# Performance work log

Hardware: AMD Instinct MI355X
Metric: run time of the kernel (lower is better)

The kernel has to match this reference:

```python
import jax, jax.numpy as jnp
import numpy as np

N = 131072   # nodes (flattened batch)
SI, VI = 128, 64   # in_dims
SO, VO = 128, 64   # out_dims
HD = 128           # h_dim


def setup_inputs() -> dict:
    key = jax.random.key(0)
    ks = jax.random.split(key, 8)
    scale = lambda fan_in: 1.0 / np.sqrt(fan_in)
    return {
        "s": jax.random.normal(ks[0], (N, SI), dtype=jnp.float32),
        "V": jax.random.normal(ks[1], (N, VI, 3), dtype=jnp.float32),
        # Linear(vi, h_dim, bias=False): weight [h_dim, vi]
        "W_h": jax.random.uniform(ks[2], (HD, VI), jnp.float32, -scale(VI), scale(VI)),
        # Linear(h_dim, vo, bias=False): weight [vo, h_dim]
        "W_V": jax.random.uniform(ks[3], (VO, HD), jnp.float32, -scale(HD), scale(HD)),
        # Linear(si + h_dim, so)
        "W_s_w": jax.random.uniform(ks[4], (SO, SI + HD), jnp.float32, -scale(SI + HD), scale(SI + HD)),
        "W_s_b": jax.random.uniform(ks[5], (SO,), jnp.float32, -scale(SI + HD), scale(SI + HD)),
        # Linear(so, vo) gate
        "W_g_w": jax.random.uniform(ks[6], (VO, SO), jnp.float32, -scale(SO), scale(SO)),
        "W_g_b": jax.random.uniform(ks[7], (VO,), jnp.float32, -scale(SO), scale(SO)),
    }


def reference(s, V, W_h, W_V, W_s_w, W_s_b, W_g_w, W_g_b):
    # Vh: contract vector-channel dim vi, keep 3 spatial dims -> [N, h_dim, 3]
    Vh = jnp.einsum("nvc,hv->nhc", V, W_h)
    # L2 norm over the 3 spatial dims -> [N, h_dim]
    Vh_norm = jnp.sqrt(jnp.sum(Vh * Vh, axis=-1))
    # V_out: [N, vo, 3]
    V_out = jnp.einsum("nhc,oh->noc", Vh, W_V)
    # scalar path: concat + linear + relu -> [N, so]
    s_cat = jnp.concatenate([s, Vh_norm], axis=-1)
    s_out = jax.nn.relu(s_cat @ W_s_w.T + W_s_b)
    # vector gate: sigmoid(Linear(s_out)) broadcast over spatial dim
    gate = jax.nn.sigmoid(s_out @ W_g_w.T + W_g_b)[..., None]  # [N, vo, 1]
    V_out = V_out * gate
    return s_out, V_out
```

## Files before the change

### kernel.cpp

```cpp
#include <hip/hip_runtime.h>
#include <hip/hip_bf16.h>
#include <math.h>

#define NNODES 131072
#define BN 32

typedef __attribute__((ext_vector_type(8))) short bf16x8;
typedef __attribute__((ext_vector_type(4))) float f32x4;

__device__ short g_w[49152];
__device__ short g_wc[4096];

__device__ __forceinline__ short f2b(float f) {
  union { float f; unsigned u; } x; x.f = f;
  unsigned r = x.u + 0x7fffu + ((x.u >> 16) & 1u);
  return (short)(r >> 16);
}
__device__ __forceinline__ short c2b(float f) {
  __hip_bfloat16 h = __float2bfloat16(f);
  return *reinterpret_cast<short*>(&h);
}

__global__ void prep_kernel(const float* __restrict__ W_h, const float* __restrict__ W_V,
                            const float* __restrict__ W_s_w, const float* __restrict__ W_g_w) {
  int b = blockIdx.x;
  if (b < 48) {
    int i4 = (b * 256 + threadIdx.x) * 4;
    const float* src;
    if (i4 < 8192)       src = W_h   + i4;
    else if (i4 < 40960) src = W_s_w + (i4 - 8192);
    else                 src = W_g_w + (i4 - 40960);
    float4 q = *(const float4*)src;
    short4 p;
    p.x = f2b(q.x); p.y = f2b(q.y); p.z = f2b(q.z); p.w = f2b(q.w);
    *(short4*)(g_w + i4) = p;
  } else {
    int gid = (b - 48) * 256 + threadIdx.x;
    int o  = gid >> 4;
    int v0 = (gid & 15) * 4;
    float a0 = 0.f, a1 = 0.f, a2 = 0.f, a3 = 0.f;
    #pragma unroll 8
    for (int h = 0; h < 128; ++h) {
      float wv = W_V[o * 128 + h];
      float4 wh = *(const float4*)(W_h + h * 64 + v0);
      a0 += wv * wh.x; a1 += wv * wh.y; a2 += wv * wh.z; a3 += wv * wh.w;
    }
    short4 p;
    p.x = f2b(a0); p.y = f2b(a1); p.z = f2b(a2); p.w = f2b(a3);
    *(short4*)(g_wc + o * 64 + v0) = p;
  }
}


__global__ __launch_bounds__(256, 3)
void gvp_kernel(const float* __restrict__ s_in, const float* __restrict__ V_in,
                const float* __restrict__ W_s_b, const float* __restrict__ W_g_b,
                float* __restrict__ s_out_g, float* __restrict__ V_out_g)
{
  __shared__ __align__(16) char smem[28672];
  char* const Vt   = smem;
  char* const VSTb = smem;
  char* const SCN  = smem + 12288;
  char* const SOUT = smem + 12288;

  const short* const g_wh = g_w;
  const short* const g_ws = g_w + 8192;
  const short* const g_wg = g_w + 40960;

  const int t    = threadIdx.x;
  const int lane = t & 63;
  const int w    = t >> 6;
  const int l15  = lane & 15;
  const int lk8  = (lane >> 4) << 3;
  const int r4   = (lane >> 4) << 2;
  const long n0  = (long)blockIdx.x * BN;

  {
    const int nl = t >> 3;
    const int vg = t & 7;
    const int v0 = vg << 3;
    const float* vp = V_in + (n0 + nl) * 192 + v0 * 3;
    float fl[24];
    #pragma unroll
    for (int i = 0; i < 6; ++i) *(float4*)(fl + 4 * i) = *(const float4*)(vp + 4 * i);
    #pragma unroll
    for (int c = 0; c < 3; ++c) {
      int row = (c << 5) + nl;
      bf16x8 p;
      #pragma unroll
      for (int j = 0; j < 8; ++j) p[j] = c2b(fl[j * 3 + c]);
      unsigned a = (unsigned)(row * 128) + (((unsigned)(v0 * 2)) ^ (unsigned)((row & 7) << 4));
      *(bf16x8*)(Vt + a) = p;
    }
  }
  {
    const int nl = t >> 3;
    const int kg = t & 7;
    const int k0 = kg << 4;
    const float* sp = s_in + (n0 + nl) * 128 + k0;
    float4 q0 = *(const float4*)(sp);
    float4 q1 = *(const float4*)(sp + 4);
    float4 q2 = *(const float4*)(sp + 8);
    float4 q3 = *(const float4*)(sp + 12);
    bf16x8 pa, pb;
    pa[0] = c2b(q0.x); pa[1] = c2b(q0.y); pa[2] = c2b(q0.z); pa[3] = c2b(q0.w);
    pa[4] = c2b(q1.x); pa[5] = c2b(q1.y); pa[6] = c2b(q1.z); pa[7] = c2b(q1.w);
    pb[0] = c2b(q2.x); pb[1] = c2b(q2.y); pb[2] = c2b(q2.z); pb[3] = c2b(q2.w);
    pb[4] = c2b(q3.x); pb[5] = c2b(q3.y); pb[6] = c2b(q3.z); pb[7] = c2b(q3.w);
    unsigned sw = (unsigned)((nl & 7) << 4);
    *(bf16x8*)(SCN + nl * 512 + (((unsigned)(k0 * 2)) ^ sw))      = pa;
    *(bf16x8*)(SCN + nl * 512 + (((unsigned)(k0 * 2 + 16)) ^ sw)) = pb;
  }
  __syncthreads();

  bf16x8 bf1[2][2];
  #pragma unroll
  for (int cc = 0; cc < 2; ++cc) {
    int h = ((2 * w + cc) << 4) + l15;
    #pragma unroll
    for (int ks = 0; ks < 2; ++ks)
      bf1[cc][ks] = *(const bf16x8*)(g_wh + h * 64 + (ks << 5) + lk8);
  }
  bf16x8 b3[8][2];
  #pragma unroll
  for (int ks = 0; ks < 8; ++ks)
    #pragma unroll
    for (int cc = 0; cc < 2; ++cc) {
      int o = (w << 5) + (cc << 4) + l15;
      b3[ks][cc] = *(const bf16x8*)(g_ws + o * 256 + (ks << 5) + lk8);
    }
  bf16x8 bc[2];
  {
    int o = (w << 4) + l15;
    bc[0] = *(const bf16x8*)(g_wc + o * 64 + lk8);
    bc[1] = *(const bf16x8*)(g_wc + o * 64 + 32 + lk8);
  }

  f32x4 acc1[6][2];
  #pragma unroll
  for (int rt = 0; rt < 6; ++rt) {
    f32x4 z = {0.f, 0.f, 0.f, 0.f};
    acc1[rt][0] = z; acc1[rt][1] = z;
  }
  #pragma unroll
  for (int rt = 0; rt < 6; ++rt) {
    int row = (rt << 4) + l15;
    unsigned sw = (unsigned)((row & 7) << 4);
    bf16x8 af0 = *(const bf16x8*)(Vt + row * 128 + (((unsigned)(lk8 * 2)) ^ sw));
    bf16x8 af1 = *(const bf16x8*)(Vt + row * 128 + (((unsigned)((32 + lk8) * 2)) ^ sw));
    #pragma unroll
    for (int cc = 0; cc < 2; ++cc) {
      acc1[rt][cc] = __builtin_amdgcn_mfma_f32_16x16x32_bf16(af0, bf1[cc][0], acc1[rt][cc], 0, 0, 0);
      acc1[rt][cc] = __builtin_amdgcn_mfma_f32_16x16x32_bf16(af1, bf1[cc][1], acc1[rt][cc], 0, 0, 0);
    }
  }

  #pragma unroll
  for (int cc = 0; cc < 2; ++cc) {
    int col = ((2 * w + cc) << 4) + l15;
    #pragma unroll
    for (int rt = 0; rt < 2; ++rt) {
      #pragma unroll
      for (int i = 0; i < 4; ++i) {
        int nl = (rt << 4) + r4 + i;
        float x0 = acc1[rt][cc][i];
        float x1 = acc1[rt + 2][cc][i];
        float x2 = acc1[rt + 4][cc][i];
        float nrm = sqrtf(x0 * x0 + x1 * x1 + x2 * x2);
        int k = 128 + col;
        unsigned a = (unsigned)(nl * 512) + (((unsigned)(k * 2)) ^ (unsigned)((nl & 7) << 4));
        *(short*)(SCN + a) = c2b(nrm);
      }
    }
  }
  __syncthreads();

  f32x4 acc3[2][2];
  {
    f32x4 z = {0.f, 0.f, 0.f, 0.f};
    acc3[0][0] = z; acc3[0][1] = z; acc3[1][0] = z; acc3[1][1] = z;
  }
  #pragma unroll
  for (int ks = 0; ks < 8; ++ks) {
    #pragma unroll
    for (int rt = 0; rt < 2; ++rt) {
      int row = (rt << 4) + l15;
      unsigned sw = (unsigned)((row & 7) << 4);
      bf16x8 a = *(const bf16x8*)(SCN + row * 512 +
                   (((unsigned)(((ks << 5) + lk8) * 2)) ^ sw));
      acc3[rt][0] = __builtin_amdgcn_mfma_f32_16x16x32_bf16(a, b3[ks][0], acc3[rt][0], 0, 0, 0);
      acc3[rt][1] = __builtin_amdgcn_mfma_f32_16x16x32_bf16(a, b3[ks][1], acc3[rt][1], 0, 0, 0);
    }
  }

  f32x4 acc2[6];
  #pragma unroll
  for (int rt = 0; rt < 6; ++rt) { f32x4 z = {0.f,0.f,0.f,0.f}; acc2[rt] = z; }
  #pragma unroll
  for (int rt = 0; rt < 6; ++rt) {
    int row = (rt << 4) + l15;
    unsigned sw = (unsigned)((row & 7) << 4);
    bf16x8 af0 = *(const bf16x8*)(Vt + row * 128 + (((unsigned)(lk8 * 2)) ^ sw));
    bf16x8 af1 = *(const bf16x8*)(Vt + row * 128 + (((unsigned)((32 + lk8) * 2)) ^ sw));
    acc2[rt] = __builtin_amdgcn_mfma_f32_16x16x32_bf16(af0, bc[0], acc2[rt], 0, 0, 0);
    acc2[rt] = __builtin_amdgcn_mfma_f32_16x16x32_bf16(af1, bc[1], acc2[rt], 0, 0, 0);
  }

  float so[2][2][4];
  {
    float bias0 = W_s_b[(w << 5) + l15];
    float bias1 = W_s_b[(w << 5) + 16 + l15];
    #pragma unroll
    for (int rt = 0; rt < 2; ++rt) {
      #pragma unroll
      for (int i = 0; i < 4; ++i) {
        int row = (rt << 4) + r4 + i;
        float v0 = fmaxf(acc3[rt][0][i] + bias0, 0.0f);
        float v1 = fmaxf(acc3[rt][1][i] + bias1, 0.0f);
        so[rt][0][i] = v0; so[rt][1][i] = v1;
        int col0 = (w << 5) + l15;
        s_out_g[(n0 + row) * 128 + col0]      = v0;
        s_out_g[(n0 + row) * 128 + col0 + 16] = v1;
      }
    }
  }
  __syncthreads();

  #pragma unroll
  for (int rt = 0; rt < 2; ++rt) {
    #pragma unroll
    for (int i = 0; i < 4; ++i) {
      int row = (rt << 4) + r4 + i;
      unsigned sw = (unsigned)((row & 7) << 4);
      int col0 = (w << 5) + l15;
      unsigned a0 = (unsigned)(row * 256) + (((unsigned)(col0 * 2)) ^ sw);
      unsigned a1 = (unsigned)(row * 256) + (((unsigned)((col0 + 16) * 2)) ^ sw);
      *(short*)(SOUT + a0) = c2b(so[rt][0][i]);
      *(short*)(SOUT + a1) = c2b(so[rt][1][i]);
    }
  }
  __syncthreads();

  f32x4 acc4[2];
  { f32x4 z = {0.f, 0.f, 0.f, 0.f}; acc4[0] = z; acc4[1] = z; }
  {
    int o = (w << 4) + l15;
    #pragma unroll
    for (int ks = 0; ks < 4; ++ks) {
      bf16x8 b4 = *(const bf16x8*)(g_wg + o * 128 + (ks << 5) + lk8);
      #pragma unroll
      for (int rt = 0; rt < 2; ++rt) {
        int row = (rt << 4) + l15;
        bf16x8 a = *(const bf16x8*)(SOUT + row * 256 +
                     (((unsigned)(((ks << 5) + lk8) * 2)) ^ ((unsigned)((row & 7) << 4))));
        acc4[rt] = __builtin_amdgcn_mfma_f32_16x16x32_bf16(a, b4, acc4[rt], 0, 0, 0);
      }
    }
  }
  float sg[2][4];
  {
    float biasg = W_g_b[(w << 4) + l15];
    #pragma unroll
    for (int nlg = 0; nlg < 2; ++nlg)
      #pragma unroll
      for (int i = 0; i < 4; ++i)
        sg[nlg][i] = 1.0f / (1.0f + __expf(-(acc4[nlg][i] + biasg)));
  }

  #pragma unroll
  for (int r = 0; r < 2; ++r) {
    {
      int col = (w << 4) + l15;
      #pragma unroll
      for (int c = 0; c < 3; ++c) {
        #pragma unroll
        for (int i = 0; i < 4; ++i) {
          int nl_rel = r4 + i;
          unsigned sw = (unsigned)(nl_rel << 4);
          unsigned base = (unsigned)(nl_rel * 768);
          *(float*)(VSTb + base + (((unsigned)((col * 3 + c) * 4)) ^ sw)) =
              acc2[c * 2 + r][i] * sg[r][i];
        }
      }
    }
    __syncthreads();
    {
      float4* Vo = (float4*)(V_out_g + (n0 + (long)(r << 4)) * 192);
      #pragma unroll
      for (int j = 0; j < 3; ++j) {
        int f = j * 256 + t;
        int nl_rel = (f * 1366) >> 16;
        int rem = f - nl_rel * 48;
        float4 q = *(const float4*)(VSTb + nl_rel * 768 +
                     (((unsigned)(rem * 16)) ^ ((unsigned)(nl_rel << 4))));
        Vo[f] = q;
      }
    }
    if (r == 0) __syncthreads();
  }
}

extern "C" void kernel_launch(void* const* d_in, const int* in_sizes, int n_in,
                              void* d_out, int out_size, void* d_ws, size_t ws_size,
                              hipStream_t stream) {
  const float* s_in  = (const float*)d_in[0];
  const float* V_in  = (const float*)d_in[1];
  const float* W_h   = (const float*)d_in[2];
  const float* W_V   = (const float*)d_in[3];
  const float* W_s_w = (const float*)d_in[4];
  const float* W_s_b = (const float*)d_in[5];
  const float* W_g_w = (const float*)d_in[6];
  const float* W_g_b = (const float*)d_in[7];
  float* out = (float*)d_out;
  float* s_out_g = out;
  float* V_out_g = out + (size_t)NNODES * 128;
  hipLaunchKernelGGL(prep_kernel, dim3(52), dim3(256), 0, stream,
                     W_h, W_V, W_s_w, W_g_w);
  hipLaunchKernelGGL(gvp_kernel, dim3(NNODES / BN), dim3(256), 0, stream,
                     s_in, V_in, W_s_b, W_g_b, s_out_g, V_out_g);
}
```

Before: 105.0 us.

## Enlarge LDS to remove barriers and stage full V tile once

```diff
diff --git a/kernel.cpp b/kernel.cpp
--- a/kernel.cpp
+++ b/kernel.cpp
@@ -57,11 +57,11 @@
                 const float* __restrict__ W_s_b, const float* __restrict__ W_g_b,
                 float* __restrict__ s_out_g, float* __restrict__ V_out_g)
 {
-  __shared__ __align__(16) char smem[28672];
-  char* const Vt   = smem;
-  char* const VSTb = smem;
-  char* const SCN  = smem + 12288;
-  char* const SOUT = smem + 12288;
+  __shared__ __align__(16) char smem[36864];
+  char*  const Vt   = smem;
+  float* const VST  = (float*)smem;
+  char*  const SCN  = smem + 12288;
+  char*  const SOUT = smem + 28672;
 
   const short* const g_wh = g_w;
   const short* const g_ws = g_w + 8192;
@@ -175,6 +175,14 @@
   }
   __syncthreads();
 
+  bf16x8 b4[4];
+  {
+    int o = (w << 4) + l15;
+    #pragma unroll
+    for (int ks = 0; ks < 4; ++ks)
+      b4[ks] = *(const bf16x8*)(g_wg + o * 128 + (ks << 5) + lk8);
+  }
+
   f32x4 acc3[2][2];
   {
     f32x4 z = {0.f, 0.f, 0.f, 0.f};
@@ -215,46 +223,30 @@
       #pragma unroll
       for (int i = 0; i < 4; ++i) {
         int row = (rt << 4) + r4 + i;
+        unsigned sw = (unsigned)((row & 7) << 4);
         float v0 = fmaxf(acc3[rt][0][i] + bias0, 0.0f);
         float v1 = fmaxf(acc3[rt][1][i] + bias1, 0.0f);
         so[rt][0][i] = v0; so[rt][1][i] = v1;
         int col0 = (w << 5) + l15;
-        s_out_g[(n0 + row) * 128 + col0]      = v0;
-        s_out_g[(n0 + row) * 128 + col0 + 16] = v1;
+        unsigned a0 = (unsigned)(row * 256) + (((unsigned)(col0 * 2)) ^ sw);
+        unsigned a1 = (unsigned)(row * 256) + (((unsigned)((col0 + 16) * 2)) ^ sw);
+        *(short*)(SOUT + a0) = c2b(v0);
+        *(short*)(SOUT + a1) = c2b(v1);
       }
-    }
-  }
-  __syncthreads();
-
-  #pragma unroll
-  for (int rt = 0; rt < 2; ++rt) {
-    #pragma unroll
-    for (int i = 0; i < 4; ++i) {
-      int row = (rt << 4) + r4 + i;
-      unsigned sw = (unsigned)((row & 7) << 4);
-      int col0 = (w << 5) + l15;
-      unsigned a0 = (unsigned)(row * 256) + (((unsigned)(col0 * 2)) ^ sw);
-      unsigned a1 = (unsigned)(row * 256) + (((unsigned)((col0 + 16) * 2)) ^ sw);
-      *(short*)(SOUT + a0) = c2b(so[rt][0][i]);
-      *(short*)(SOUT + a1) = c2b(so[rt][1][i]);
     }
   }
   __syncthreads();
 
   f32x4 acc4[2];
   { f32x4 z = {0.f, 0.f, 0.f, 0.f}; acc4[0] = z; acc4[1] = z; }
-  {
-    int o = (w << 4) + l15;
-    #pragma unroll
-    for (int ks = 0; ks < 4; ++ks) {
-      bf16x8 b4 = *(const bf16x8*)(g_wg + o * 128 + (ks << 5) + lk8);
-      #pragma unroll
-      for (int rt = 0; rt < 2; ++rt) {
-        int row = (rt << 4) + l15;
-        bf16x8 a = *(const bf16x8*)(SOUT + row * 256 +
-                     (((unsigned)(((ks << 5) + lk8) * 2)) ^ ((unsigned)((row & 7) << 4))));
-        acc4[rt] = __builtin_amdgcn_mfma_f32_16x16x32_bf16(a, b4, acc4[rt], 0, 0, 0);
-      }
+  #pragma unroll
+  for (int ks = 0; ks < 4; ++ks) {
+    #pragma unroll
+    for (int rt = 0; rt < 2; ++rt) {
+      int row = (rt << 4) + l15;
+      bf16x8 a = *(const bf16x8*)(SOUT + row * 256 +
+                   (((unsigned)(((ks << 5) + lk8) * 2)) ^ ((unsigned)((row & 7) << 4))));
+      acc4[rt] = __builtin_amdgcn_mfma_f32_16x16x32_bf16(a, b4[ks], acc4[rt], 0, 0, 0);
     }
   }
   float sg[2][4];
@@ -267,36 +259,41 @@
         sg[nlg][i] = 1.0f / (1.0f + __expf(-(acc4[nlg][i] + biasg)));
   }
 
-  #pragma unroll
-  for (int r = 0; r < 2; ++r) {
-    {
-      int col = (w << 4) + l15;
-      #pragma unroll
-      for (int c = 0; c < 3; ++c) {
-        #pragma unroll
-        for (int i = 0; i < 4; ++i) {
-          int nl_rel = r4 + i;
-          unsigned sw = (unsigned)(nl_rel << 4);
-          unsigned base = (unsigned)(nl_rel * 768);
-          *(float*)(VSTb + base + (((unsigned)((col * 3 + c) * 4)) ^ sw)) =
-              acc2[c * 2 + r][i] * sg[r][i];
-        }
+  {
+    int col = (w << 4) + l15;
+    #pragma unroll
+    for (int rt = 0; rt < 6; ++rt) {
+      int c   = rt >> 1;
+      int nlg = rt & 1;
+      #pragma unroll
+      for (int i = 0; i < 4; ++i) {
+        int nl = (nlg << 4) + r4 + i;
+        VST[nl * 192 + col * 3 + c] = acc2[rt][i] * sg[nlg][i];
       }
     }
-    __syncthreads();
-    {
-      float4* Vo = (float4*)(V_out_g + (n0 + (long)(r << 4)) * 192);
-      #pragma unroll
-      for (int j = 0; j < 3; ++j) {
-        int f = j * 256 + t;
-        int nl_rel = (f * 1366) >> 16;
-        int rem = f - nl_rel * 48;
-        float4 q = *(const float4*)(VSTb + nl_rel * 768 +
-                     (((unsigned)(rem * 16)) ^ ((unsigned)(nl_rel << 4))));
-        Vo[f] = q;
+  }
+  __syncthreads();
+
+  {
+    float4* Vo = (float4*)(V_out_g + n0 * 192);
+    const float4* Vs = (const float4*)VST;
+    #pragma unroll
+    for (int i = 0; i < 6; ++i) {
+      int idx = t + 256 * i;
+      Vo[idx] = Vs[idx];
+    }
+  }
+  {
+    int col0 = (w << 5) + l15;
+    #pragma unroll
+    for (int rt = 0; rt < 2; ++rt) {
+      #pragma unroll
+      for (int i = 0; i < 4; ++i) {
+        int row = (rt << 4) + r4 + i;
+        s_out_g[(n0 + row) * 128 + col0]      = so[rt][0][i];
+        s_out_g[(n0 + row) * 128 + col0 + 16] = so[rt][1][i];
       }
     }
-    if (r == 0) __syncthreads();
   }
 }
 
```

New measurement: 102.9 us. -2.0%, faster.
